# Performance work log

Measured on AMD Instinct MI355X. Metric: run time of the kernel, lower is better.

## Reference

```python
import jax, jax.numpy as jnp
import numpy as np

H = 64
NUM_HEADS = 4
NUM_LAYERS = 2
B = 524288
EPS = 1e-5


def _layernorm(x, g, b):
    mu = jnp.mean(x, axis=-1, keepdims=True)
    var = jnp.mean((x - mu) ** 2, axis=-1, keepdims=True)
    return (x - mu) * jax.lax.rsqrt(var + EPS) * g + b


def _mha(x, w_qkv, b_qkv, w_o, b_o):
    # x: (B, M, H). Fused in-proj like torch nn.MultiheadAttention.
    Bx, M, Hx = x.shape
    hd = Hx // NUM_HEADS
    qkv = x @ w_qkv.T + b_qkv                      # (B, M, 3H)
    q, k, v = jnp.split(qkv, 3, axis=-1)
    q = q.reshape(Bx, M, NUM_HEADS, hd)
    k = k.reshape(Bx, M, NUM_HEADS, hd)
    v = v.reshape(Bx, M, NUM_HEADS, hd)
    scores = jnp.einsum('bqnd,bknd->bnqk', q, k) / jnp.sqrt(jnp.asarray(hd, x.dtype))
    a = jax.nn.softmax(scores, axis=-1)
    o = jnp.einsum('bnqk,bknd->bqnd', a, v).reshape(Bx, M, Hx)
    return o @ w_o.T + b_o


def _block(x, rel, p):
    attn_out = _mha(x, p['w_qkv'], p['b_qkv'], p['w_o'], p['b_o'])
    attn_out = attn_out * rel[:, :, None]
    x = _layernorm(x + attn_out, p['n1_g'], p['n1_b'])
    ffn = jax.nn.relu(x @ p['ffn_w'].T + p['ffn_b'])
    return _layernorm(x + ffn, p['n2_g'], p['n2_b'])


def setup_inputs() -> dict:
    key = jax.random.key(0)
    ks = jax.random.split(key, 32)
    inp = {
        'h_poi': jax.random.normal(ks[0], (B, H), jnp.float32),
        'h_census': jax.random.normal(ks[1], (B, H), jnp.float32),
        'h_traffic': jax.random.normal(ks[2], (B, H), jnp.float32),
        'mfr_poi': jax.random.uniform(ks[3], (B, 2), jnp.float32),
        'mfr_census': jax.random.uniform(ks[4], (B, 2), jnp.float32),
        'mfr_traffic': jax.random.uniform(ks[5], (B, 2), jnp.float32),
        'rel_w': jax.random.normal(ks[6], (1, 2), jnp.float32) * 0.5,
        'rel_b': jnp.zeros((1,), jnp.float32),
    }
    s = 1.0 / np.sqrt(H)
    for l in range(NUM_LAYERS):
        kk = jax.random.split(ks[7 + l], 6)
        inp[f'l{l}_w_qkv'] = jax.random.normal(kk[0], (3 * H, H), jnp.float32) * s
        inp[f'l{l}_b_qkv'] = jnp.zeros((3 * H,), jnp.float32)
        inp[f'l{l}_w_o'] = jax.random.normal(kk[1], (H, H), jnp.float32) * s
        inp[f'l{l}_b_o'] = jnp.zeros((H,), jnp.float32)
        inp[f'l{l}_ffn_w'] = jax.random.normal(kk[2], (H, H), jnp.float32) * s
        inp[f'l{l}_ffn_b'] = jnp.zeros((H,), jnp.float32)
        inp[f'l{l}_n1_g'] = jnp.ones((H,), jnp.float32)
        inp[f'l{l}_n1_b'] = jnp.zeros((H,), jnp.float32)
        inp[f'l{l}_n2_g'] = jnp.ones((H,), jnp.float32)
        inp[f'l{l}_n2_b'] = jnp.zeros((H,), jnp.float32)
    return inp


def reference(h_poi, h_census, h_traffic, mfr_poi, mfr_census, mfr_traffic,
              rel_w, rel_b,
              l0_w_qkv, l0_b_qkv, l0_w_o, l0_b_o, l0_ffn_w, l0_ffn_b,
              l0_n1_g, l0_n1_b, l0_n2_g, l0_n2_b,
              l1_w_qkv, l1_b_qkv, l1_w_o, l1_b_o, l1_ffn_w, l1_ffn_b,
              l1_n1_g, l1_n1_b, l1_n2_g, l1_n2_b):
    x = jnp.stack([h_poi, h_census, h_traffic], axis=1)  # (B, 3, H)
    rel = jax.nn.sigmoid(
        jnp.stack([mfr_poi, mfr_census, mfr_traffic], axis=1) @ rel_w.T + rel_b
    )[..., 0]                                            # (B, 3)
    layers = [
        dict(w_qkv=l0_w_qkv, b_qkv=l0_b_qkv, w_o=l0_w_o, b_o=l0_b_o,
             ffn_w=l0_ffn_w, ffn_b=l0_ffn_b, n1_g=l0_n1_g, n1_b=l0_n1_b,
             n2_g=l0_n2_g, n2_b=l0_n2_b),
        dict(w_qkv=l1_w_qkv, b_qkv=l1_b_qkv, w_o=l1_w_o, b_o=l1_b_o,
             ffn_w=l1_ffn_w, ffn_b=l1_ffn_b, n1_g=l1_n1_g, n1_b=l1_n1_b,
             n2_g=l1_n2_g, n2_b=l1_n2_b),
    ]
    for p in layers:
        x = _block(x, rel, p)
    return x  # (B, 3, H); slice [:, i, :] per modality if dict output desired
```

## Files before the change

### kernel.cpp

```cpp
#include <hip/hip_runtime.h>

typedef unsigned short u16;
typedef unsigned int u32;
typedef _Float16 h16;
typedef h16 h2v __attribute__((ext_vector_type(2)));
typedef h16 v8h __attribute__((ext_vector_type(8)));
typedef float v4f __attribute__((ext_vector_type(4)));

#define ROWS_PB 16
#define TOK 48
#define XS 76
#define QS 196
#define WS_L 20480

struct Params {
  const float *h0, *h1, *h2;
  const float *m0, *m1, *m2;
  const float *relw, *relb;
  const float *b_qkv[2], *b_o[2], *b_f[2];
  const float *n1g[2], *n1b[2], *n2g[2], *n2b[2];
  const u16* ws;
  float* out;
};

__device__ __forceinline__ u16 f2h(float f){ union{h16 h; u16 u;} c; c.h = (h16)f; return c.u; }

union Frag { uint2 u2[2]; uint4 u4; v8h v; };
union V16h { uint2 u2[4]; h2v h[8]; h16 s[16]; };
union U2H  { uint2 u; h16 s[4]; };

#if __has_builtin(__builtin_amdgcn_fdot2)
#define FDOT2(a,b,c) __builtin_amdgcn_fdot2((a),(b),(c),false)
#else
#define FDOT2(a,b,c) ((float)(a)[0]*(float)(b)[0] + (float)(a)[1]*(float)(b)[1] + (c))
#endif

__global__ __launch_bounds__(256, 2)
void prep_w(const float* wq0, const float* wo0, const float* wf0,
            const float* wq1, const float* wo1, const float* wf1, u16* ws){
  int idx = blockIdx.x * 256 + threadIdx.x;
  if (idx >= 2 * WS_L) return;
  int l = idx / WS_L, rem = idx % WS_L;
  const float* W; int loc;
  if (rem < 12288)      { W = l ? wq1 : wq0; loc = rem; }
  else if (rem < 16384) { W = l ? wo1 : wo0; loc = rem - 12288; }
  else                  { W = l ? wf1 : wf0; loc = rem - 16384; }
  int e = loc & 7, lane = (loc >> 3) & 63, fk = loc >> 9;
  int kk = fk & 1, nt = fk >> 1;
  int k = kk * 32 + 4 * (lane >> 4) + (e & 3) + (e >> 2) * 16;
  int n = nt * 16 + (lane & 15);
  ws[idx] = f2h(W[n * 64 + k]);
}

__device__ __forceinline__ v8h ldA(const u16* ap){
  Frag f;
  f.u2[0] = *(const uint2*)(ap);
  f.u2[1] = *(const uint2*)(ap + 16);
  return f.v;
}
__device__ __forceinline__ void ld16(V16h& o, const u16* p){
#pragma unroll
  for (int i = 0; i < 4; ++i) o.u2[i] = *(const uint2*)(p + 4 * i);
}

__global__ __launch_bounds__(192, 4)
void inter_encoder(Params p){
  __shared__ u16  sX[TOK * XS];
  __shared__ u16  sQKV[TOK * QS];
  __shared__ float sRel[TOK];

  const int tid  = threadIdx.x;
  const int lane = tid & 63, wv = tid >> 6;
  const int n15  = lane & 15, g = lane >> 4;
  const long long rowBase = (long long)blockIdx.x * ROWS_PB;

#pragma unroll
  for (int it = 0; it < 4; ++it){
    int idx = it * 192 + tid;
    int t = idx >> 4, c4 = (idx & 15) * 4;
    int r = t / 3, m = t - 3 * r;
    const float* hp = (m == 0) ? p.h0 : (m == 1) ? p.h1 : p.h2;
    float4 vv = *(const float4*)(hp + (rowBase + r) * 64 + c4);
    u32 lo = (u32)f2h(vv.x) | ((u32)f2h(vv.y) << 16);
    u32 hi = (u32)f2h(vv.z) | ((u32)f2h(vv.w) << 16);
    *(uint2*)(sX + t * XS + c4) = make_uint2(lo, hi);
  }
  if (tid < TOK){
    int t = tid, r = t / 3, m = t - 3 * r;
    const float* mf = (m == 0) ? p.m0 : (m == 1) ? p.m1 : p.m2;
    float a0 = mf[(rowBase + r) * 2 + 0], a1 = mf[(rowBase + r) * 2 + 1];
    float z = a0 * p.relw[0] + a1 * p.relw[1] + p.relb[0];
    sRel[t] = 1.f / (1.f + __expf(-z));
  }
  __syncthreads();

  for (int l = 0; l < 2; ++l){
    const u16* wsl = p.ws + l * WS_L;

    Frag aq[4][2];
    v4f bq4[4];
#pragma unroll
    for (int j = 0; j < 4; ++j){
      int mt = 4 * wv + j;
      aq[j][0].u4 = *(const uint4*)(wsl + ((mt * 2 + 0) * 64 + lane) * 8);
      aq[j][1].u4 = *(const uint4*)(wsl + ((mt * 2 + 1) * 64 + lane) * 8);
      bq4[j] = *(const v4f*)(p.b_qkv[l] + 16 * mt + 4 * g);
    }
#pragma unroll
    for (int nt = 0; nt < 3; ++nt){
      const u16* bp = sX + (16 * nt + n15) * XS + 4 * g;
      v8h b0 = ldA(bp), b1 = ldA(bp + 32);
#pragma unroll
      for (int j = 0; j < 4; ++j){
        v4f acc = bq4[j];
        acc = __builtin_amdgcn_mfma_f32_16x16x32_f16(aq[j][0].v, b0, acc, 0, 0, 0);
        acc = __builtin_amdgcn_mfma_f32_16x16x32_f16(aq[j][1].v, b1, acc, 0, 0, 0);
        u32 lo = (u32)f2h(acc[0]) | ((u32)f2h(acc[1]) << 16);
        u32 hi = (u32)f2h(acc[2]) | ((u32)f2h(acc[3]) << 16);
        *(uint2*)(sQKV + (16 * nt + n15) * QS + 16 * (4 * wv + j) + 4 * g)
            = make_uint2(lo, hi);
      }
    }
    __syncthreads();

    {
      const int t1 = wv, r = lane >> 2, h = lane & 3;
      const u16* base = sQKV + (3 * r) * QS + 16 * h;
      V16h q, k0, k1, k2;
      ld16(q,  base + t1 * QS);
      ld16(k0, base + 64);
      ld16(k1, base + QS + 64);
      ld16(k2, base + 2 * QS + 64);
      float s0 = 0.f, s1 = 0.f, s2 = 0.f;
#pragma unroll
      for (int pp = 0; pp < 8; ++pp){
        s0 = FDOT2(q.h[pp], k0.h[pp], s0);
        s1 = FDOT2(q.h[pp], k1.h[pp], s1);
        s2 = FDOT2(q.h[pp], k2.h[pp], s2);
      }
      s0 *= 0.25f; s1 *= 0.25f; s2 *= 0.25f;
      float mx = fmaxf(fmaxf(s0, s1), s2);
      float e0 = __expf(s0 - mx), e1 = __expf(s1 - mx), e2 = __expf(s2 - mx);
      float inv = 1.f / (e0 + e1 + e2);
      h16 w0 = (h16)(e0 * inv), w1 = (h16)(e1 * inv), w2 = (h16)(e2 * inv);
      h2v aw0 = {w0, w0}, aw1 = {w1, w1}, aw2 = {w2, w2};
      V16h v0, v1, v2, o;
      ld16(v0, base + 128);
      ld16(v1, base + QS + 128);
      ld16(v2, base + 2 * QS + 128);
#pragma unroll
      for (int pp = 0; pp < 8; ++pp)
        o.h[pp] = aw0 * v0.h[pp] + aw1 * v1.h[pp] + aw2 * v2.h[pp];
      u16* op = sQKV + (3 * r + t1) * QS + 16 * h;
#pragma unroll
      for (int pp = 0; pp < 4; ++pp) *(uint2*)(op + 4 * pp) = o.u2[pp];
    }
    __syncthreads();

    {
      const int trow = 16 * wv + n15;
      const float relt = sRel[trow];
      const u16* bp = sQKV + trow * QS + 4 * g;
      v8h b0 = ldA(bp), b1 = ldA(bp + 32);

      float val[4][4];
      float psum = 0.f;
#pragma unroll
      for (int j = 0; j < 4; ++j){
        Frag a0, a1;
        a0.u4 = *(const uint4*)(wsl + 12288 + ((j * 2 + 0) * 64 + lane) * 8);
        a1.u4 = *(const uint4*)(wsl + 12288 + ((j * 2 + 1) * 64 + lane) * 8);
        v4f acc = *(const v4f*)(p.b_o[l] + 16 * j + 4 * g);
        acc = __builtin_amdgcn_mfma_f32_16x16x32_f16(a0.v, b0, acc, 0, 0, 0);
        acc = __builtin_amdgcn_mfma_f32_16x16x32_f16(a1.v, b1, acc, 0, 0, 0);
        U2H x; x.u = *(const uint2*)(sX + trow * XS + 16 * j + 4 * g);
#pragma unroll
        for (int i = 0; i < 4; ++i){
          val[j][i] = acc[i] * relt + (float)x.s[i];
          psum += val[j][i];
        }
      }
      psum += __shfl_xor(psum, 16, 64);
      psum += __shfl_xor(psum, 32, 64);
      float mu = psum * (1.f / 64.f);
      float vs = 0.f;
#pragma unroll
      for (int j = 0; j < 4; ++j)
#pragma unroll
        for (int i = 0; i < 4; ++i){ float d = val[j][i] - mu; vs += d * d; }
      vs += __shfl_xor(vs, 16, 64);
      vs += __shfl_xor(vs, 32, 64);
      float rs = rsqrtf(vs * (1.f / 64.f) + 1e-5f);

      float y[4][4];
#pragma unroll
      for (int j = 0; j < 4; ++j){
        v4f gg = *(const v4f*)(p.n1g[l] + 16 * j + 4 * g);
        v4f bb = *(const v4f*)(p.n1b[l] + 16 * j + 4 * g);
#pragma unroll
        for (int i = 0; i < 4; ++i) y[j][i] = (val[j][i] - mu) * rs * gg[i] + bb[i];
        u32 lo = (u32)f2h(y[j][0]) | ((u32)f2h(y[j][1]) << 16);
        u32 hi = (u32)f2h(y[j][2]) | ((u32)f2h(y[j][3]) << 16);
        *(uint2*)(sX + trow * XS + 16 * j + 4 * g) = make_uint2(lo, hi);
      }

      const u16* ap2 = sX + trow * XS + 4 * g;
      v8h c0 = ldA(ap2), c1 = ldA(ap2 + 32);

      float psum2 = 0.f;
#pragma unroll
      for (int j = 0; j < 4; ++j){
        Frag a0, a1;
        a0.u4 = *(const uint4*)(wsl + 16384 + ((j * 2 + 0) * 64 + lane) * 8);
        a1.u4 = *(const uint4*)(wsl + 16384 + ((j * 2 + 1) * 64 + lane) * 8);
        v4f acc = *(const v4f*)(p.b_f[l] + 16 * j + 4 * g);
        acc = __builtin_amdgcn_mfma_f32_16x16x32_f16(a0.v, c0, acc, 0, 0, 0);
        acc = __builtin_amdgcn_mfma_f32_16x16x32_f16(a1.v, c1, acc, 0, 0, 0);
#pragma unroll
        for (int i = 0; i < 4; ++i){
          float v2 = y[j][i] + fmaxf(acc[i], 0.f);
          val[j][i] = v2;
          psum2 += v2;
        }
      }
      psum2 += __shfl_xor(psum2, 16, 64);
      psum2 += __shfl_xor(psum2, 32, 64);
      float mu2 = psum2 * (1.f / 64.f);
      float vs2 = 0.f;
#pragma unroll
      for (int j = 0; j < 4; ++j)
#pragma unroll
        for (int i = 0; i < 4; ++i){ float d = val[j][i] - mu2; vs2 += d * d; }
      vs2 += __shfl_xor(vs2, 16, 64);
      vs2 += __shfl_xor(vs2, 32, 64);
      float rs2 = rsqrtf(vs2 * (1.f / 64.f) + 1e-5f);

      if (l == 0){
#pragma unroll
        for (int j = 0; j < 4; ++j){
          v4f gg = *(const v4f*)(p.n2g[0] + 16 * j + 4 * g);
          v4f bb = *(const v4f*)(p.n2b[0] + 16 * j + 4 * g);
          float z0 = (val[j][0] - mu2) * rs2 * gg[0] + bb[0];
          float z1 = (val[j][1] - mu2) * rs2 * gg[1] + bb[1];
          float z2 = (val[j][2] - mu2) * rs2 * gg[2] + bb[2];
          float z3 = (val[j][3] - mu2) * rs2 * gg[3] + bb[3];
          u32 lo = (u32)f2h(z0) | ((u32)f2h(z1) << 16);
          u32 hi = (u32)f2h(z2) | ((u32)f2h(z3) << 16);
          *(uint2*)(sX + trow * XS + 16 * j + 4 * g) = make_uint2(lo, hi);
        }
      } else {
        float* op = p.out + (rowBase * 3 + trow) * 64;
#pragma unroll
        for (int j = 0; j < 4; ++j){
          v4f gg = *(const v4f*)(p.n2g[1] + 16 * j + 4 * g);
          v4f bb = *(const v4f*)(p.n2b[1] + 16 * j + 4 * g);
          v4f yo;
#pragma unroll
          for (int i = 0; i < 4; ++i) yo[i] = (val[j][i] - mu2) * rs2 * gg[i] + bb[i];
          *(v4f*)(op + 16 * j + 4 * g) = yo;
        }
      }
    }
    __syncthreads();
  }
}

extern "C" void kernel_launch(void* const* d_in, const int* in_sizes, int n_in,
                              void* d_out, int out_size, void* d_ws, size_t ws_size,
                              hipStream_t stream){
  const float* const* in = (const float* const*)d_in;
  u16* ws = (u16*)d_ws;

  prep_w<<<(2 * WS_L + 255) / 256, 256, 0, stream>>>(
      in[8], in[10], in[12], in[18], in[20], in[22], ws);

  Params p;
  p.h0 = in[0]; p.h1 = in[1]; p.h2 = in[2];
  p.m0 = in[3]; p.m1 = in[4]; p.m2 = in[5];
  p.relw = in[6]; p.relb = in[7];
  for (int l = 0; l < 2; ++l){
    int b = 8 + 10 * l;
    p.b_qkv[l] = in[b + 1];
    p.b_o[l]   = in[b + 3];
    p.b_f[l]   = in[b + 5];
    p.n1g[l]   = in[b + 6]; p.n1b[l] = in[b + 7];
    p.n2g[l]   = in[b + 8]; p.n2b[l] = in[b + 9];
  }
  p.ws = ws;
  p.out = (float*)d_out;

  const int nblk = 524288 / ROWS_PB;
  inter_encoder<<<nblk, 192, 0, stream>>>(p);
}
```

Measured before the change: 444.5 us.

## Compute attention in registers from QKV MFMA outputs, dropping QKV shared buffer

Reorders tokens modality-major and gives each of four waves one head, so that wave's Q, K and V tiles for all three modalities stay in MFMA accumulators. Scores and softmax are then computed with cross-lane shuffles, and only the attention output goes to a smaller shared buffer. This removes the large QKV shared-memory round trip and one barrier, and raises the block to 256 threads. In exchange, the fourth wave sits idle during the out-projection and FFN phases, and the extra accumulators raise register pressure.

Result: slower. 459.7 us (+3.4%).

```diff
diff --git a/kernel.cpp b/kernel.cpp
--- a/kernel.cpp
+++ b/kernel.cpp
@@ -3,14 +3,13 @@
 typedef unsigned short u16;
 typedef unsigned int u32;
 typedef _Float16 h16;
-typedef h16 h2v __attribute__((ext_vector_type(2)));
 typedef h16 v8h __attribute__((ext_vector_type(8)));
 typedef float v4f __attribute__((ext_vector_type(4)));
 
 #define ROWS_PB 16
 #define TOK 48
 #define XS 76
-#define QS 196
+#define AS 70
 #define WS_L 20480
 
 struct Params {
@@ -26,14 +25,7 @@
 __device__ __forceinline__ u16 f2h(float f){ union{h16 h; u16 u;} c; c.h = (h16)f; return c.u; }
 
 union Frag { uint2 u2[2]; uint4 u4; v8h v; };
-union V16h { uint2 u2[4]; h2v h[8]; h16 s[16]; };
 union U2H  { uint2 u; h16 s[4]; };
-
-#if __has_builtin(__builtin_amdgcn_fdot2)
-#define FDOT2(a,b,c) __builtin_amdgcn_fdot2((a),(b),(c),false)
-#else
-#define FDOT2(a,b,c) ((float)(a)[0]*(float)(b)[0] + (float)(a)[1]*(float)(b)[1] + (c))
-#endif
 
 __global__ __launch_bounds__(256, 2)
 void prep_w(const float* wq0, const float* wo0, const float* wf0,
@@ -58,15 +50,11 @@
   f.u2[1] = *(const uint2*)(ap + 16);
   return f.v;
 }
-__device__ __forceinline__ void ld16(V16h& o, const u16* p){
-#pragma unroll
-  for (int i = 0; i < 4; ++i) o.u2[i] = *(const uint2*)(p + 4 * i);
-}
-
-__global__ __launch_bounds__(192, 4)
+
+__global__ __launch_bounds__(256, 5)
 void inter_encoder(Params p){
   __shared__ u16  sX[TOK * XS];
-  __shared__ u16  sQKV[TOK * QS];
+  __shared__ u16  sATT[TOK * AS];
   __shared__ float sRel[TOK];
 
   const int tid  = threadIdx.x;
@@ -75,10 +63,10 @@
   const long long rowBase = (long long)blockIdx.x * ROWS_PB;
 
 #pragma unroll
-  for (int it = 0; it < 4; ++it){
-    int idx = it * 192 + tid;
+  for (int it = 0; it < 3; ++it){
+    int idx = it * 256 + tid;
     int t = idx >> 4, c4 = (idx & 15) * 4;
-    int r = t / 3, m = t - 3 * r;
+    int m = t >> 4, r = t & 15;
     const float* hp = (m == 0) ? p.h0 : (m == 1) ? p.h1 : p.h2;
     float4 vv = *(const float4*)(hp + (rowBase + r) * 64 + c4);
     u32 lo = (u32)f2h(vv.x) | ((u32)f2h(vv.y) << 16);
@@ -86,81 +74,72 @@
     *(uint2*)(sX + t * XS + c4) = make_uint2(lo, hi);
   }
   if (tid < TOK){
-    int t = tid, r = t / 3, m = t - 3 * r;
+    int m = tid >> 4, r = tid & 15;
     const float* mf = (m == 0) ? p.m0 : (m == 1) ? p.m1 : p.m2;
     float a0 = mf[(rowBase + r) * 2 + 0], a1 = mf[(rowBase + r) * 2 + 1];
     float z = a0 * p.relw[0] + a1 * p.relw[1] + p.relb[0];
-    sRel[t] = 1.f / (1.f + __expf(-z));
+    sRel[tid] = 1.f / (1.f + __expf(-z));
   }
   __syncthreads();
 
   for (int l = 0; l < 2; ++l){
     const u16* wsl = p.ws + l * WS_L;
 
-    Frag aq[4][2];
-    v4f bq4[4];
-#pragma unroll
-    for (int j = 0; j < 4; ++j){
-      int mt = 4 * wv + j;
-      aq[j][0].u4 = *(const uint4*)(wsl + ((mt * 2 + 0) * 64 + lane) * 8);
-      aq[j][1].u4 = *(const uint4*)(wsl + ((mt * 2 + 1) * 64 + lane) * 8);
-      bq4[j] = *(const v4f*)(p.b_qkv[l] + 16 * mt + 4 * g);
-    }
-#pragma unroll
-    for (int nt = 0; nt < 3; ++nt){
-      const u16* bp = sX + (16 * nt + n15) * XS + 4 * g;
+    Frag aq[3][2];
+    v4f bq4[3];
+#pragma unroll
+    for (int c = 0; c < 3; ++c){
+      int mt = 4 * c + wv;
+      aq[c][0].u4 = *(const uint4*)(wsl + ((mt * 2 + 0) * 64 + lane) * 8);
+      aq[c][1].u4 = *(const uint4*)(wsl + ((mt * 2 + 1) * 64 + lane) * 8);
+      bq4[c] = *(const v4f*)(p.b_qkv[l] + 16 * mt + 4 * g);
+    }
+    v4f acc[3][3];
+#pragma unroll
+    for (int m = 0; m < 3; ++m){
+      const u16* bp = sX + (16 * m + n15) * XS + 4 * g;
       v8h b0 = ldA(bp), b1 = ldA(bp + 32);
 #pragma unroll
-      for (int j = 0; j < 4; ++j){
-        v4f acc = bq4[j];
-        acc = __builtin_amdgcn_mfma_f32_16x16x32_f16(aq[j][0].v, b0, acc, 0, 0, 0);
-        acc = __builtin_amdgcn_mfma_f32_16x16x32_f16(aq[j][1].v, b1, acc, 0, 0, 0);
-        u32 lo = (u32)f2h(acc[0]) | ((u32)f2h(acc[1]) << 16);
-        u32 hi = (u32)f2h(acc[2]) | ((u32)f2h(acc[3]) << 16);
-        *(uint2*)(sQKV + (16 * nt + n15) * QS + 16 * (4 * wv + j) + 4 * g)
-            = make_uint2(lo, hi);
-      }
+      for (int c = 0; c < 3; ++c){
+        acc[c][m] = bq4[c];
+        acc[c][m] = __builtin_amdgcn_mfma_f32_16x16x32_f16(aq[c][0].v, b0, acc[c][m], 0, 0, 0);
+        acc[c][m] = __builtin_amdgcn_mfma_f32_16x16x32_f16(aq[c][1].v, b1, acc[c][m], 0, 0, 0);
+      }
+    }
+
+    float s[3][3];
+#pragma unroll
+    for (int m1 = 0; m1 < 3; ++m1)
+#pragma unroll
+      for (int m2 = 0; m2 < 3; ++m2){
+        float pp = acc[0][m1][0] * acc[1][m2][0]
+                 + acc[0][m1][1] * acc[1][m2][1]
+                 + acc[0][m1][2] * acc[1][m2][2]
+                 + acc[0][m1][3] * acc[1][m2][3];
+        pp += __shfl_xor(pp, 16, 64);
+        pp += __shfl_xor(pp, 32, 64);
+        s[m1][m2] = pp * 0.25f;
+      }
+#pragma unroll
+    for (int m1 = 0; m1 < 3; ++m1){
+      float mx = fmaxf(fmaxf(s[m1][0], s[m1][1]), s[m1][2]);
+      float e0 = __expf(s[m1][0] - mx), e1 = __expf(s[m1][1] - mx), e2 = __expf(s[m1][2] - mx);
+      float inv = 1.f / (e0 + e1 + e2);
+      float a0 = e0 * inv, a1 = e1 * inv, a2 = e2 * inv;
+      float o0 = a0 * acc[2][0][0] + a1 * acc[2][1][0] + a2 * acc[2][2][0];
+      float o1 = a0 * acc[2][0][1] + a1 * acc[2][1][1] + a2 * acc[2][2][1];
+      float o2 = a0 * acc[2][0][2] + a1 * acc[2][1][2] + a2 * acc[2][2][2];
+      float o3 = a0 * acc[2][0][3] + a1 * acc[2][1][3] + a2 * acc[2][2][3];
+      u32 lo = (u32)f2h(o0) | ((u32)f2h(o1) << 16);
+      u32 hi = (u32)f2h(o2) | ((u32)f2h(o3) << 16);
+      *(uint2*)(sATT + (16 * m1 + n15) * AS + 16 * wv + 4 * g) = make_uint2(lo, hi);
     }
     __syncthreads();
 
-    {
-      const int t1 = wv, r = lane >> 2, h = lane & 3;
-      const u16* base = sQKV + (3 * r) * QS + 16 * h;
-      V16h q, k0, k1, k2;
-      ld16(q,  base + t1 * QS);
-      ld16(k0, base + 64);
-      ld16(k1, base + QS + 64);
-      ld16(k2, base + 2 * QS + 64);
-      float s0 = 0.f, s1 = 0.f, s2 = 0.f;
-#pragma unroll
-      for (int pp = 0; pp < 8; ++pp){
-        s0 = FDOT2(q.h[pp], k0.h[pp], s0);
-        s1 = FDOT2(q.h[pp], k1.h[pp], s1);
-        s2 = FDOT2(q.h[pp], k2.h[pp], s2);
-      }
-      s0 *= 0.25f; s1 *= 0.25f; s2 *= 0.25f;
-      float mx = fmaxf(fmaxf(s0, s1), s2);
-      float e0 = __expf(s0 - mx), e1 = __expf(s1 - mx), e2 = __expf(s2 - mx);
-      float inv = 1.f / (e0 + e1 + e2);
-      h16 w0 = (h16)(e0 * inv), w1 = (h16)(e1 * inv), w2 = (h16)(e2 * inv);
-      h2v aw0 = {w0, w0}, aw1 = {w1, w1}, aw2 = {w2, w2};
-      V16h v0, v1, v2, o;
-      ld16(v0, base + 128);
-      ld16(v1, base + QS + 128);
-      ld16(v2, base + 2 * QS + 128);
-#pragma unroll
-      for (int pp = 0; pp < 8; ++pp)
-        o.h[pp] = aw0 * v0.h[pp] + aw1 * v1.h[pp] + aw2 * v2.h[pp];
-      u16* op = sQKV + (3 * r + t1) * QS + 16 * h;
-#pragma unroll
-      for (int pp = 0; pp < 4; ++pp) *(uint2*)(op + 4 * pp) = o.u2[pp];
-    }
-    __syncthreads();
-
-    {
+    if (wv < 3){
       const int trow = 16 * wv + n15;
       const float relt = sRel[trow];
-      const u16* bp = sQKV + trow * QS + 4 * g;
+      const u16* bp = sATT + trow * AS + 4 * g;
       v8h b0 = ldA(bp), b1 = ldA(bp + 32);
 
       float val[4][4];
@@ -170,13 +149,13 @@
         Frag a0, a1;
         a0.u4 = *(const uint4*)(wsl + 12288 + ((j * 2 + 0) * 64 + lane) * 8);
         a1.u4 = *(const uint4*)(wsl + 12288 + ((j * 2 + 1) * 64 + lane) * 8);
-        v4f acc = *(const v4f*)(p.b_o[l] + 16 * j + 4 * g);
-        acc = __builtin_amdgcn_mfma_f32_16x16x32_f16(a0.v, b0, acc, 0, 0, 0);
-        acc = __builtin_amdgcn_mfma_f32_16x16x32_f16(a1.v, b1, acc, 0, 0, 0);
+        v4f acc2 = *(const v4f*)(p.b_o[l] + 16 * j + 4 * g);
+        acc2 = __builtin_amdgcn_mfma_f32_16x16x32_f16(a0.v, b0, acc2, 0, 0, 0);
+        acc2 = __builtin_amdgcn_mfma_f32_16x16x32_f16(a1.v, b1, acc2, 0, 0, 0);
         U2H x; x.u = *(const uint2*)(sX + trow * XS + 16 * j + 4 * g);
 #pragma unroll
         for (int i = 0; i < 4; ++i){
-          val[j][i] = acc[i] * relt + (float)x.s[i];
+          val[j][i] = acc2[i] * relt + (float)x.s[i];
           psum += val[j][i];
         }
       }
@@ -213,12 +192,12 @@
         Frag a0, a1;
         a0.u4 = *(const uint4*)(wsl + 16384 + ((j * 2 + 0) * 64 + lane) * 8);
         a1.u4 = *(const uint4*)(wsl + 16384 + ((j * 2 + 1) * 64 + lane) * 8);
-        v4f acc = *(const v4f*)(p.b_f[l] + 16 * j + 4 * g);
-        acc = __builtin_amdgcn_mfma_f32_16x16x32_f16(a0.v, c0, acc, 0, 0, 0);
-        acc = __builtin_amdgcn_mfma_f32_16x16x32_f16(a1.v, c1, acc, 0, 0, 0);
+        v4f acc2 = *(const v4f*)(p.b_f[l] + 16 * j + 4 * g);
+        acc2 = __builtin_amdgcn_mfma_f32_16x16x32_f16(a0.v, c0, acc2, 0, 0, 0);
+        acc2 = __builtin_amdgcn_mfma_f32_16x16x32_f16(a1.v, c1, acc2, 0, 0, 0);
 #pragma unroll
         for (int i = 0; i < 4; ++i){
-          float v2 = y[j][i] + fmaxf(acc[i], 0.f);
+          float v2 = y[j][i] + fmaxf(acc2[i], 0.f);
           val[j][i] = v2;
           psum2 += v2;
         }
@@ -249,7 +228,7 @@
           *(uint2*)(sX + trow * XS + 16 * j + 4 * g) = make_uint2(lo, hi);
         }
       } else {
-        float* op = p.out + (rowBase * 3 + trow) * 64;
+        float* op = p.out + ((rowBase + n15) * 3 + wv) * 64;
 #pragma unroll
         for (int j = 0; j < 4; ++j){
           v4f gg = *(const v4f*)(p.n2g[1] + 16 * j + 4 * g);
@@ -290,5 +269,5 @@
   p.out = (float*)d_out;
 
   const int nblk = 524288 / ROWS_PB;
-  inter_encoder<<<nblk, 192, 0, stream>>>(p);
-}
+  inter_encoder<<<nblk, 256, 0, stream>>>(p);
+}
```
